# Performance work log

Measured on AMD Instinct MI355X. Metric: run time of the kernel, lower is better.

Reference implementation:

```python
import jax, jax.numpy as jnp
import numpy as np

SCALE = 1.0 / 16.0      # spatial scale: image coords -> feature-map coords (stride-16 backbone)
OUT = 7                 # roi_pool_outsize
RATIO = 2               # sampling_ratio
NUM_CLASSES = 21
HID = 1024
SCORE_THRESH = 0.05
NMS_THRESH = 0.5
DET = 100               # detections_per_img
MIN_SIZE = 0.01
LOG_MAX = float(np.log(1000.0 / 16.0))  # standard bbox decode dw/dh clamp


def _bilinear(feat, ys, xs):
    # feat [C,H,W]; ys [Py], xs [Px] -> [C,Py,Px] (torchvision roi_align interpolation, aligned=False)
    C, H, W = feat.shape
    vy = (ys > -1.0) & (ys < H)
    vx = (xs > -1.0) & (xs < W)
    y = jnp.clip(ys, 0.0, H - 1.0)
    x = jnp.clip(xs, 0.0, W - 1.0)
    y0 = jnp.floor(y).astype(jnp.int32)
    x0 = jnp.floor(x).astype(jnp.int32)
    y1 = jnp.minimum(y0 + 1, H - 1)
    x1 = jnp.minimum(x0 + 1, W - 1)
    ly = (y - y0)[:, None]
    lx = (x - x0)[None, :]
    f00 = feat[:, y0[:, None], x0[None, :]]
    f01 = feat[:, y0[:, None], x1[None, :]]
    f10 = feat[:, y1[:, None], x0[None, :]]
    f11 = feat[:, y1[:, None], x1[None, :]]
    val = (f00 * (1.0 - ly) * (1.0 - lx) + f01 * (1.0 - ly) * lx
           + f10 * ly * (1.0 - lx) + f11 * ly * lx)
    return val * (vy[:, None] & vx[None, :])


def _roi_align(features, boxes, bidx):
    # features [N,C,H,W], boxes [R,4] (image coords), bidx [R] -> [R,C,OUT,OUT]
    N, C, H, W = features.shape
    b = boxes * SCALE
    rw = jnp.maximum(b[:, 2] - b[:, 0], 1.0)
    rh = jnp.maximum(b[:, 3] - b[:, 1], 1.0)
    bw = rw / OUT
    bh = rh / OUT
    # per-bin sample offsets: (ph + (i+0.5)/ratio) for ph in [0,OUT), i in [0,RATIO)
    g = (jnp.arange(OUT, dtype=jnp.float32)[:, None]
         + (jnp.arange(RATIO, dtype=jnp.float32)[None, :] + 0.5) / RATIO).reshape(-1)  # [OUT*RATIO]
    ys = b[:, 1][:, None] + g[None, :] * bh[:, None]  # [R, OUT*RATIO]
    xs = b[:, 0][:, None] + g[None, :] * bw[:, None]
    vals = jax.vmap(lambda i, yr, xr: _bilinear(features[i], yr, xr))(bidx, ys, xs)  # [R,C,P,P]
    R = boxes.shape[0]
    return vals.reshape(R, C, OUT, RATIO, OUT, RATIO).mean(axis=(3, 5))


def _decode(deltas, props):
    # deltas [R,K,4], props [R,4]; weights (10,10,5,5) as in the module
    pw = props[:, 2] - props[:, 0]
    ph = props[:, 3] - props[:, 1]
    pcx = props[:, 0] + 0.5 * pw
    pcy = props[:, 1] + 0.5 * ph
    dx = deltas[..., 0] / 10.0
    dy = deltas[..., 1] / 10.0
    dw = jnp.minimum(deltas[..., 2] / 5.0, LOG_MAX)
    dh = jnp.minimum(deltas[..., 3] / 5.0, LOG_MAX)
    cx = dx * pw[:, None] + pcx[:, None]
    cy = dy * ph[:, None] + pcy[:, None]
    w = jnp.exp(dw) * pw[:, None]
    h = jnp.exp(dh) * ph[:, None]
    return jnp.stack([cx - 0.5 * w, cy - 0.5 * h, cx + 0.5 * w, cy + 0.5 * h], axis=-1)


def _per_image(scores, boxes, img):
    # scores [S,K], boxes [S,K,4]. Drop background class, flatten, filter, class-aware NMS, top-DET.
    S, K = scores.shape
    sc = scores[:, 1:].reshape(-1)                 # [M]
    bx = boxes[:, 1:, :].reshape(-1, 4)            # [M,4]
    lb = jnp.broadcast_to(jnp.arange(1, K, dtype=jnp.int32)[None, :], (S, K - 1)).reshape(-1)
    wv = bx[:, 2] - bx[:, 0]
    hv = bx[:, 3] - bx[:, 1]
    valid = (sc > SCORE_THRESH) & (wv >= MIN_SIZE) & (hv >= MIN_SIZE)
    live0 = jnp.where(valid, sc, -1.0)
    # batched_nms via per-class coordinate offsets
    nb = bx + (lb.astype(bx.dtype) * (img + 1.0))[:, None]
    areas = (nb[:, 2] - nb[:, 0]) * (nb[:, 3] - nb[:, 1])

    def step(live, _):
        i = jnp.argmax(live)
        s = live[i]
        b = nb[i]
        xx1 = jnp.maximum(b[0], nb[:, 0])
        yy1 = jnp.maximum(b[1], nb[:, 1])
        xx2 = jnp.minimum(b[2], nb[:, 2])
        yy2 = jnp.minimum(b[3], nb[:, 3])
        inter = jnp.maximum(xx2 - xx1, 0.0) * jnp.maximum(yy2 - yy1, 0.0)
        area_i = (b[2] - b[0]) * (b[3] - b[1])
        iou = inter / (area_i + areas - inter + 1e-9)
        live = jnp.where(iou > NMS_THRESH, -1.0, live)  # also suppresses i itself (iou=1)
        return live, (i, s)

    _, (idxs, svals) = jax.lax.scan(step, live0, None, length=DET)
    keep = svals > SCORE_THRESH
    out_boxes = jnp.where(keep[:, None], bx[idxs], 0.0)
    out_scores = jnp.where(keep, svals, 0.0)
    out_labels = jnp.where(keep, lb[idxs], 0)
    return out_boxes, out_scores, out_labels


def _forward(features, proposals, w1, b1, w2, b2, wc, bc, wb, bb, image_size):
    N, C, H, W = features.shape
    S = proposals.shape[1]
    props = proposals.reshape(-1, 4)
    bidx = jnp.repeat(jnp.arange(N), S)
    feats = _roi_align(features, props, bidx)          # [R,C,7,7]
    x = feats.reshape(N * S, -1)                       # [R, C*49]
    h = jax.nn.relu(x @ w1 + b1)
    h = jax.nn.relu(h @ w2 + b2)
    cls = h @ wc + bc                                  # [R,K]
    deltas = (h @ wb + bb).reshape(N * S, NUM_CLASSES, 4)
    scores = jax.nn.softmax(cls, axis=-1)
    boxes = _decode(deltas, props)                     # [R,K,4]
    img = float(image_size)
    boxes = jnp.clip(boxes, 0.0, img)                  # square image -> clip both coords to [0,img]
    scores = scores.reshape(N, S, NUM_CLASSES)
    boxes = boxes.reshape(N, S, NUM_CLASSES, 4)
    return jax.vmap(lambda s, bx: _per_image(s, bx, img))(scores, boxes)


def setup_inputs() -> dict:
    key = jax.random.key(0)
    ks = jax.random.split(key, 12)
    N, S, C, H, W = 2, 512, 512, 50, 50
    IMG = 800
    features = jax.random.normal(ks[0], (N, C, H, W), jnp.float32)
    x1 = jax.random.uniform(ks[1], (N, S)) * (IMG - 80.0)
    y1 = jax.random.uniform(ks[2], (N, S)) * (IMG - 80.0)
    x2 = jnp.minimum(x1 + 16.0 + jax.random.uniform(ks[3], (N, S)) * 180.0, float(IMG))
    y2 = jnp.minimum(y1 + 16.0 + jax.random.uniform(ks[4], (N, S)) * 180.0, float(IMG))
    proposals = jnp.stack([x1, y1, x2, y2], axis=-1)
    D = C * OUT * OUT  # 25088
    w1 = jax.random.normal(ks[5], (D, HID), jnp.float32) * 0.01
    b1 = jnp.zeros((HID,), jnp.float32)
    w2 = jax.random.normal(ks[6], (HID, HID), jnp.float32) * 0.02
    b2 = jnp.zeros((HID,), jnp.float32)
    wc = jax.random.normal(ks[7], (HID, NUM_CLASSES), jnp.float32) * 0.05
    bc = jnp.zeros((NUM_CLASSES,), jnp.float32)
    wb = jax.random.normal(ks[8], (HID, NUM_CLASSES * 4), jnp.float32) * 0.02
    bb = jnp.zeros((NUM_CLASSES * 4,), jnp.float32)
    return {"features": features, "proposals": proposals, "w1": w1, "b1": b1,
            "w2": w2, "b2": b2, "wc": wc, "bc": bc, "wb": wb, "bb": bb,
            "image_size": IMG}


def reference(features, proposals, w1, b1, w2, b2, wc, bc, wb, bb, image_size):
    boxes, scores, labels = _forward(features, proposals, w1, b1, w2, b2, wc, bc, wb, bb, image_size)
    return boxes, scores, labels
```

## Files before the change

kernel.cpp:

```cpp
#include <hip/hip_runtime.h>
#include <cmath>

#define NIMG 2
#define SPROP 512
#define NROI 1024
#define CCH 512
#define FH 50
#define FW 50
#define K1 25088
#define HID 1024
#define NCLS 21
#define NDET 100
#define IMGSZ 800.0f
#define LOGMAX 4.135166556742356f
#define MCAND 10240
#define ZSPLIT 8
#define KCHUNK 3136
#define ZSPLIT2 8
#define KCHUNK2 128

typedef unsigned short u16;
typedef __attribute__((ext_vector_type(8))) short short8;
typedef __attribute__((ext_vector_type(4))) float f32x4;
typedef __attribute__((ext_vector_type(16))) float f32x16;

__device__ __forceinline__ u16 f2bf(float x) {
  unsigned int u = __float_as_uint(x);
  u += 0x7fffu + ((u >> 16) & 1u);
  return (u16)(u >> 16);
}
__device__ __forceinline__ float bf2f(u16 h) {
  return __uint_as_float(((unsigned int)h) << 16);
}

__device__ __forceinline__ void gld16(const u16* g, u16* l) {
  __builtin_amdgcn_global_load_lds(
      (const __attribute__((address_space(1))) void*)g,
      (__attribute__((address_space(3))) void*)l, 16, 0, 0);
}

template <bool BF16OUT>
__global__ __launch_bounds__(256) void roi_kernel(
    const float* __restrict__ feat, const float* __restrict__ props,
    float* __restrict__ X, u16* __restrict__ Xhi, u16* __restrict__ Xlo) {
  const int r = blockIdx.x;
  const int n = r >> 9;
  const int tid = threadIdx.x;
  __shared__ float tile[32 * 273 + 16];
  __shared__ float4 ymeta[14];
  __shared__ float4 xmeta[14];
  __shared__ int smin[2];

  const float p0 = props[r * 4 + 0] * 0.0625f;
  const float p1 = props[r * 4 + 1] * 0.0625f;
  const float p2 = props[r * 4 + 2] * 0.0625f;
  const float p3 = props[r * 4 + 3] * 0.0625f;
  const float bw = fmaxf(p2 - p0, 1.0f) / 7.0f;
  const float bh = fmaxf(p3 - p1, 1.0f) / 7.0f;

  if (tid < 14) {
    const int j = tid;
    const float g = (float)(j >> 1) + ((float)(j & 1) + 0.5f) * 0.5f;
    const float y = p1 + g * bh;
    const float vy = (y > -1.0f && y < (float)FH) ? 0.5f : 0.0f;
    const float yc = fminf(fmaxf(y, 0.0f), (float)(FH - 1));
    const int y0 = (int)floorf(yc);
    const int y1 = min(y0 + 1, FH - 1);
    const float ly = yc - (float)y0;
    const float yc0 = fminf(fmaxf(p1 + 0.25f * bh, 0.0f), (float)(FH - 1));
    const int ymin = (int)floorf(yc0);
    float4 m;
    m.x = __int_as_float((y0 - ymin) * 17);
    m.y = __int_as_float((y1 - ymin) * 17);
    m.z = (1.0f - ly) * vy;
    m.w = ly * vy;
    ymeta[j] = m;
    if (j == 0) smin[0] = ymin;
  } else if (tid >= 16 && tid < 30) {
    const int j = tid - 16;
    const float g = (float)(j >> 1) + ((float)(j & 1) + 0.5f) * 0.5f;
    const float x = p0 + g * bw;
    const float vx = (x > -1.0f && x < (float)FW) ? 0.5f : 0.0f;
    const float xc = fminf(fmaxf(x, 0.0f), (float)(FW - 1));
    const int x0 = (int)floorf(xc);
    const int x1 = min(x0 + 1, FW - 1);
    const float lx = xc - (float)x0;
    const float xc0 = fminf(fmaxf(p0 + 0.25f * bw, 0.0f), (float)(FW - 1));
    const int xmin = (int)floorf(xc0);
    const float wx0 = (1.0f - lx) * vx;
    const float wx1 = lx * vx;
    const int d = x1 - x0;
    float4 m;
    m.x = __int_as_float(x0 - xmin);
    m.y = wx0 + (d ? 0.0f : wx1);
    m.z = d ? wx1 : 0.0f;
    m.w = 0.0f;
    xmeta[j] = m;
    if (j == 0) smin[1] = xmin;
  }
  __syncthreads();

  const int ymin = smin[0], xmin = smin[1];
  const float* fb = feat + (size_t)n * CCH * (FH * FW);
  const int gy = min(ymin + (tid >> 4), FH - 1);
  const int gx = min(xmin + (tid & 15), FW - 1);
  const int offp = gy * FW + gx;
  const int wslot = (tid >> 4) * 17 + (tid & 15);
  const int q = tid & 7;
  const int c = tid >> 3;
  const int cb = c * 273;

  float pf[32];
#pragma unroll
  for (int e = 0; e < 32; ++e) pf[e] = fb[(size_t)e * (FH * FW) + offp];

  for (int cc = 0; cc < 16; ++cc) {
#pragma unroll
    for (int e = 0; e < 32; ++e) tile[e * 273 + wslot] = pf[e];
    __syncthreads();
    if (cc < 15) {
      const float* fb2 = fb + (size_t)(cc + 1) * 32 * (FH * FW);
#pragma unroll
      for (int e = 0; e < 32; ++e) pf[e] = fb2[(size_t)e * (FH * FW) + offp];
    }
#pragma unroll
    for (int jj = 0; jj < 7; ++jj) {
      const int s = q + (jj << 3);
      if (s < 49) {
        const int oy = s / 7;
        const int ox = s - oy * 7;
        const float4 ym0 = ymeta[2 * oy];
        const float4 ym1 = ymeta[2 * oy + 1];
        const float4 xm0 = xmeta[2 * ox];
        const float4 xm1 = xmeta[2 * ox + 1];
        float acc = 0.0f;
#pragma unroll
        for (int sy = 0; sy < 2; ++sy) {
          const float4 ym = sy ? ym1 : ym0;
          const int ro0 = cb + __float_as_int(ym.x);
          const int ro1 = cb + __float_as_int(ym.y);
#pragma unroll
          for (int sx = 0; sx < 2; ++sx) {
            const float4 xm = sx ? xm1 : xm0;
            const int px = __float_as_int(xm.x);
            const float a0 = tile[ro0 + px];
            const float a1 = tile[ro0 + px + 1];
            const float b0 = tile[ro1 + px];
            const float b1 = tile[ro1 + px + 1];
            acc += ym.z * (xm.y * a0 + xm.z * a1) +
                   ym.w * (xm.y * b0 + xm.z * b1);
          }
        }
        const size_t k = (size_t)r * K1 + (size_t)(cc * 32 + c) * 49 + s;
        if (BF16OUT) {
          const u16 h = f2bf(acc);
          Xhi[k] = h;
          Xlo[k] = f2bf(acc - bf2f(h));
        } else {
          X[k] = acc;
        }
      }
    }
    __syncthreads();
  }
}

template <int KDIM>
__global__ __launch_bounds__(256) void convw_kernel(
    const float* __restrict__ w, u16* __restrict__ Wh, u16* __restrict__ Wl) {
  __shared__ u16 sh[64][65], sl[64][65];
  const int k0 = blockIdx.x * 64;
  const int n0 = blockIdx.y * 64;
  const int t = threadIdx.x;
#pragma unroll
  for (int e = 0; e < 16; ++e) {
    const int idx = t + e * 256;
    const int kl = idx >> 6, nl = idx & 63;
    const float v = w[(size_t)(k0 + kl) * HID + n0 + nl];
    const u16 h = f2bf(v);
    sh[kl][nl] = h;
    sl[kl][nl] = f2bf(v - bf2f(h));
  }
  __syncthreads();
#pragma unroll
  for (int e = 0; e < 16; ++e) {
    const int idx = t + e * 256;
    const int nl = idx >> 6, kl = idx & 63;
    Wh[(size_t)(n0 + nl) * KDIM + k0 + kl] = sh[kl][nl];
    Wl[(size_t)(n0 + nl) * KDIM + k0 + kl] = sl[kl][nl];
  }
}

template <int KS, int KCH, bool SWZ>
__global__ __launch_bounds__(512, 2) void gemm_mfma_split(
    const u16* __restrict__ Ahg, const u16* __restrict__ Alg,
    const u16* __restrict__ Bhg, const u16* __restrict__ Blg,
    float* __restrict__ CP) {
  __shared__ u16 Ah[2][128][32], Al[2][128][32];
  __shared__ u16 Bh[2][256][32], Bl[2][256][32];
  const int tid = threadIdx.x;
  const int lane = tid & 63;
  const int wv = tid >> 6;
  const int wm = (wv >> 2) << 6;
  const int wn = (wv & 3) << 6;

  int bx = blockIdx.x, by = blockIdx.y, bz = blockIdx.z;
  if (SWZ) {
    const int f = blockIdx.x + ((blockIdx.y + (blockIdx.z << 3)) << 2);
    bz = f & 7;
    const int u = f >> 3;
    bx = u & 3;
    by = u >> 2;
  }
  const int mT = by << 7;
  const int nT = bx << 8;
  const int kz = bz * KCH;
  constexpr int NSTEP = KCH / 32;

  const int sr = tid >> 2;
  const int sqw = (((tid & 3) ^ ((tid >> 3) & 3)) << 3);
  const size_t aoff  = (size_t)(mT + sr) * KS + sqw;
  const size_t b0off = (size_t)(nT + sr) * KS + sqw;
  const size_t b1off = (size_t)(nT + sr + 128) * KS + sqw;
  const int lofs = tid * 8;

  f32x16 acc[2][2];
#pragma unroll
  for (int i = 0; i < 2; ++i)
#pragma unroll
    for (int j = 0; j < 2; ++j)
#pragma unroll
      for (int e = 0; e < 16; ++e) acc[i][j][e] = 0.0f;

  const int fm = lane & 31;
  const int fh = lane >> 5;
  const int vswz = (fm >> 1) & 3;

  auto stage = [&](int buf, int kb) {
    gld16(Ahg + aoff + kb, &Ah[buf][0][0] + lofs);
    gld16(Alg + aoff + kb, &Al[buf][0][0] + lofs);
    gld16(Bhg + b0off + kb, &Bh[buf][0][0] + lofs);
    gld16(Bhg + b1off + kb, &Bh[buf][128][0] + lofs);
    gld16(Blg + b0off + kb, &Bl[buf][0][0] + lofs);
    gld16(Blg + b1off + kb, &Bl[buf][128][0] + lofs);
  };

  auto compute = [&](int buf) {
#pragma unroll
    for (int kh = 0; kh < 2; ++kh) {
      const int cA = ((((kh << 1) | fh) ^ vswz) << 3);
      short8 fa_h[2], fa_l[2], fb_h[2], fb_l[2];
#pragma unroll
      for (int t = 0; t < 2; ++t) {
        fa_h[t] = *(const short8*)(&Ah[buf][wm + t * 32 + fm][cA]);
        fa_l[t] = *(const short8*)(&Al[buf][wm + t * 32 + fm][cA]);
        fb_h[t] = *(const short8*)(&Bh[buf][wn + t * 32 + fm][cA]);
        fb_l[t] = *(const short8*)(&Bl[buf][wn + t * 32 + fm][cA]);
      }
#pragma unroll
      for (int ti = 0; ti < 2; ++ti)
#pragma unroll
        for (int tj = 0; tj < 2; ++tj) {
          acc[ti][tj] = __builtin_amdgcn_mfma_f32_32x32x16_bf16(
              fa_h[ti], fb_h[tj], acc[ti][tj], 0, 0, 0);
          acc[ti][tj] = __builtin_amdgcn_mfma_f32_32x32x16_bf16(
              fa_h[ti], fb_l[tj], acc[ti][tj], 0, 0, 0);
          acc[ti][tj] = __builtin_amdgcn_mfma_f32_32x32x16_bf16(
              fa_l[ti], fb_h[tj], acc[ti][tj], 0, 0, 0);
        }
    }
  };

  stage(0, kz);
  asm volatile("s_waitcnt vmcnt(0)" ::: "memory");
  __builtin_amdgcn_s_barrier();
  __builtin_amdgcn_sched_barrier(0);

  int cur = 0;
  for (int s = 0; s < NSTEP; ++s) {
    if (s + 1 < NSTEP) {
      stage(cur ^ 1, kz + (s + 1) * 32);
      asm volatile("s_waitcnt vmcnt(6)" ::: "memory");
    } else {
      asm volatile("s_waitcnt vmcnt(0)" ::: "memory");
    }
    __builtin_amdgcn_s_barrier();
    __builtin_amdgcn_sched_barrier(0);
    compute(cur);
    __builtin_amdgcn_sched_barrier(0);
    __builtin_amdgcn_s_barrier();
    cur ^= 1;
  }

  float* Cp = CP + (size_t)bz * ((size_t)NROI * HID);
  const int ccol = nT + wn + fm;
  const int rbase = mT + wm + (fh << 2);
#pragma unroll
  for (int ti = 0; ti < 2; ++ti)
#pragma unroll
    for (int tj = 0; tj < 2; ++tj)
#pragma unroll
      for (int rg = 0; rg < 16; ++rg) {
        const int row = rbase + ti * 32 + (rg & 3) + 8 * (rg >> 2);
        Cp[(size_t)row * HID + ccol + tj * 32] = acc[ti][tj][rg];
      }
}

__global__ __launch_bounds__(256) void gemm1_kernel(
    const float* __restrict__ A, const float* __restrict__ B,
    float* __restrict__ CP) {
  __shared__ float As[16][68];
  __shared__ float Bs[16][68];
  const int tid = threadIdx.x;
  const int mTile = blockIdx.y << 6;
  const int nTile = blockIdx.x << 6;
  const int k0 = blockIdx.z * KCHUNK;
  const int ty = tid >> 4, tx = tid & 15;
  const int ar = tid >> 2, ac = (tid & 3) << 2;
  const int br = tid >> 4, bcl = (tid & 15) << 2;
  float acc[4][4] = {};

  for (int kb = k0; kb < k0 + KCHUNK; kb += 16) {
    const float4 av = *(const float4*)(A + (size_t)(mTile + ar) * K1 + kb + ac);
    const float4 bv = *(const float4*)(B + (size_t)(kb + br) * HID + nTile + bcl);
    As[ac + 0][ar] = av.x; As[ac + 1][ar] = av.y;
    As[ac + 2][ar] = av.z; As[ac + 3][ar] = av.w;
    *(float4*)(&Bs[br][bcl]) = bv;
    __syncthreads();
#pragma unroll
    for (int kk = 0; kk < 16; ++kk) {
      const float4 a4 = *(const float4*)(&As[kk][ty << 2]);
      const float4 b4 = *(const float4*)(&Bs[kk][tx << 2]);
      const float aa[4] = {a4.x, a4.y, a4.z, a4.w};
      const float bb4[4] = {b4.x, b4.y, b4.z, b4.w};
#pragma unroll
      for (int i = 0; i < 4; ++i)
#pragma unroll
        for (int j = 0; j < 4; ++j)
          acc[i][j] = fmaf(aa[i], bb4[j], acc[i][j]);
    }
    __syncthreads();
  }
  float* Cp = CP + (size_t)blockIdx.z * (HID * NROI);
#pragma unroll
  for (int i = 0; i < 4; ++i) {
    *(float4*)(Cp + (size_t)(mTile + (ty << 2) + i) * HID + nTile + (tx << 2)) =
        make_float4(acc[i][0], acc[i][1], acc[i][2], acc[i][3]);
  }
}

__global__ __launch_bounds__(256) void bias_relu_bf16_kernel(
    const float* __restrict__ CP, const float* __restrict__ b1,
    u16* __restrict__ H1h, u16* __restrict__ H1l) {
  const int idx = blockIdx.x * 256 + threadIdx.x;
  float v = b1[idx & (HID - 1)];
#pragma unroll
  for (int z = 0; z < ZSPLIT; ++z) v += CP[(size_t)z * (HID * NROI) + idx];
  v = fmaxf(v, 0.0f);
  const u16 h = f2bf(v);
  H1h[idx] = h;
  H1l[idx] = f2bf(v - bf2f(h));
}

__global__ __launch_bounds__(256) void bias_relu_f32_kernel(
    const float* __restrict__ CP, const float* __restrict__ b1,
    float* __restrict__ H1) {
  const int idx = blockIdx.x * 256 + threadIdx.x;
  float v = b1[idx & (HID - 1)];
#pragma unroll
  for (int z = 0; z < ZSPLIT; ++z) v += CP[(size_t)z * (HID * NROI) + idx];
  H1[idx] = fmaxf(v, 0.0f);
}

__global__ __launch_bounds__(256) void bias_relu2_kernel(
    const float* __restrict__ CP2, const float* __restrict__ b2,
    float* __restrict__ H2) {
  const int idx = blockIdx.x * 256 + threadIdx.x;
  float v = b2[idx & (HID - 1)];
#pragma unroll
  for (int z = 0; z < ZSPLIT2; ++z) v += CP2[(size_t)z * (HID * NROI) + idx];
  H2[idx] = fmaxf(v, 0.0f);
}

__global__ __launch_bounds__(256) void gemm2_kernel(
    const float* __restrict__ A, const float* __restrict__ B,
    const float* __restrict__ bias, float* __restrict__ C) {
  __shared__ float As[16][68];
  __shared__ float Bs[16][68];
  const int tid = threadIdx.x;
  const int mTile = blockIdx.y << 6;
  const int nTile = blockIdx.x << 6;
  const int ty = tid >> 4, tx = tid & 15;
  const int ar = tid >> 2, ac = (tid & 3) << 2;
  const int br = tid >> 4, bcl = (tid & 15) << 2;
  float acc[4][4] = {};

  for (int kb = 0; kb < HID; kb += 16) {
    const float4 av = *(const float4*)(A + (size_t)(mTile + ar) * HID + kb + ac);
    const float4 bv = *(const float4*)(B + (size_t)(kb + br) * HID + nTile + bcl);
    As[ac + 0][ar] = av.x; As[ac + 1][ar] = av.y;
    As[ac + 2][ar] = av.z; As[ac + 3][ar] = av.w;
    *(float4*)(&Bs[br][bcl]) = bv;
    __syncthreads();
#pragma unroll
    for (int kk = 0; kk < 16; ++kk) {
      const float4 a4 = *(const float4*)(&As[kk][ty << 2]);
      const float4 b4 = *(const float4*)(&Bs[kk][tx << 2]);
      const float aa[4] = {a4.x, a4.y, a4.z, a4.w};
      const float bb4[4] = {b4.x, b4.y, b4.z, b4.w};
#pragma unroll
      for (int i = 0; i < 4; ++i)
#pragma unroll
        for (int j = 0; j < 4; ++j)
          acc[i][j] = fmaf(aa[i], bb4[j], acc[i][j]);
    }
    __syncthreads();
  }
#pragma unroll
  for (int i = 0; i < 4; ++i) {
#pragma unroll
    for (int j = 0; j < 4; ++j) {
      float v = acc[i][j] + bias[nTile + (tx << 2) + j];
      acc[i][j] = fmaxf(v, 0.0f);
    }
    *(float4*)(C + (size_t)(mTile + (ty << 2) + i) * HID + nTile + (tx << 2)) =
        make_float4(acc[i][0], acc[i][1], acc[i][2], acc[i][3]);
  }
}

__global__ __launch_bounds__(128) void heads_kernel(
    const float* __restrict__ H2m, const float* __restrict__ wc,
    const float* __restrict__ bc, const float* __restrict__ wb,
    const float* __restrict__ bb, const float* __restrict__ props,
    float* __restrict__ BX2, float* __restrict__ NB2,
    float* __restrict__ LV2) {
  const int r = blockIdx.x;
  const int tid = threadIdx.x;
  __shared__ float hrow[HID];
  __shared__ float vals[112];
  __shared__ float red[2];

  for (int i = tid; i < HID; i += 128) hrow[i] = H2m[(size_t)r * HID + i];
  __syncthreads();

  if (tid < 105) {
    float acc;
    if (tid < NCLS) {
      acc = bc[tid];
      for (int kk = 0; kk < HID; ++kk) acc = fmaf(hrow[kk], wc[kk * NCLS + tid], acc);
    } else {
      const int j = tid - NCLS;
      acc = bb[j];
      for (int kk = 0; kk < HID; ++kk) acc = fmaf(hrow[kk], wb[kk * (NCLS * 4) + j], acc);
    }
    vals[tid] = acc;
  }
  __syncthreads();

  if (tid == 0) {
    float m = vals[0];
    for (int k = 1; k < NCLS; ++k) m = fmaxf(m, vals[k]);
    float s = 0.0f;
    for (int k = 0; k < NCLS; ++k) s += expf(vals[k] - m);
    red[0] = m;
    red[1] = 1.0f / s;
  }
  __syncthreads();

  if (tid >= 1 && tid <= 20) {
    const int k = tid;
    const float prob = expf(vals[k] - red[0]) * red[1];

    const float px1 = props[r * 4 + 0], py1 = props[r * 4 + 1];
    const float px2 = props[r * 4 + 2], py2 = props[r * 4 + 3];
    const float pw = px2 - px1, ph = py2 - py1;
    const float pcx = px1 + 0.5f * pw, pcy = py1 + 0.5f * ph;

    const float dx = vals[NCLS + k * 4 + 0] / 10.0f;
    const float dy = vals[NCLS + k * 4 + 1] / 10.0f;
    const float dw = fminf(vals[NCLS + k * 4 + 2] / 5.0f, LOGMAX);
    const float dh = fminf(vals[NCLS + k * 4 + 3] / 5.0f, LOGMAX);

    const float cx = dx * pw + pcx, cy = dy * ph + pcy;
    const float w = expf(dw) * pw, h = expf(dh) * ph;
    float b0 = cx - 0.5f * w, b1c = cy - 0.5f * h;
    float b2 = cx + 0.5f * w, b3 = cy + 0.5f * h;
    b0 = fminf(fmaxf(b0, 0.0f), IMGSZ);
    b1c = fminf(fmaxf(b1c, 0.0f), IMGSZ);
    b2 = fminf(fmaxf(b2, 0.0f), IMGSZ);
    b3 = fminf(fmaxf(b3, 0.0f), IMGSZ);

    const float wv = b2 - b0, hv = b3 - b1c;
    const bool valid = (prob > 0.05f) && (wv >= 0.01f) && (hv >= 0.01f);

    const int n = r >> 9, s = r & 511;
    const int cand = (k - 1) * SPROP + s;
    const size_t bi = (size_t)n * MCAND + cand;
    const float off = (float)k * (IMGSZ + 1.0f);

    BX2[bi * 4 + 0] = b0; BX2[bi * 4 + 1] = b1c;
    BX2[bi * 4 + 2] = b2; BX2[bi * 4 + 3] = b3;
    NB2[bi * 4 + 0] = b0 + off; NB2[bi * 4 + 1] = b1c + off;
    NB2[bi * 4 + 2] = b2 + off; NB2[bi * 4 + 3] = b3 + off;
    LV2[bi] = valid ? prob : -1.0f;
  }
}

template <int CTRL>
__device__ __forceinline__ void red2(float& v, int& ix) {
  const float tv = __int_as_float(__builtin_amdgcn_update_dpp(
      (int)0xC0000000, __float_as_int(v), CTRL, 0xf, 0xf, false));
  const int ti = __builtin_amdgcn_update_dpp(0x7fffffff, ix, CTRL, 0xf, 0xf, false);
  if (tv > v || (tv == v && ti < ix)) { v = tv; ix = ti; }
}
__device__ __forceinline__ void wave_red2(float& v, int& ix) {
  red2<0x111>(v, ix);
  red2<0x112>(v, ix);
  red2<0x114>(v, ix);
  red2<0x118>(v, ix);
  red2<0x142>(v, ix);
  red2<0x143>(v, ix);
}

__global__ __launch_bounds__(64) void nms_class_kernel(
    const float* __restrict__ NB2, const float* __restrict__ LV2,
    float* __restrict__ ksg, int* __restrict__ kig, int* __restrict__ cntg) {
  const int bid = blockIdx.x;
  const int lane = threadIdx.x;
  __shared__ float4 lbox[SPROP];
  const size_t cb = (size_t)bid * SPROP;

  float lv[8], b0[8], b1[8], b2[8], b3[8], ar[8];
#pragma unroll
  for (int j = 0; j < 8; ++j) {
    const int s = lane + j * 64;
    lv[j] = LV2[cb + s];
    const float4 b = *(const float4*)(NB2 + (cb + s) * 4);
    b0[j] = b.x; b1[j] = b.y; b2[j] = b.z; b3[j] = b.w;
    ar[j] = (b.z - b.x) * (b.w - b.y);
    lbox[s] = b;
  }

  int cnt = 0;
  for (int d = 0; d < NDET; ++d) {
    float bv = -2.0f;
    int bix = 0x7fffffff;
#pragma unroll
    for (int j = 0; j < 8; ++j) {
      if (lv[j] > bv) { bv = lv[j]; bix = lane + j * 64; }
    }
    wave_red2(bv, bix);
    const float bv2 = __shfl(bv, 63);
    const int bix2 = __shfl(bix, 63);
    if (bv2 <= 0.05f) break;

    if (lane == 0) {
      ksg[bid * NDET + cnt] = bv2;
      kig[bid * NDET + cnt] = bix2;
    }
    ++cnt;

    const float4 wb = lbox[bix2];
    const float wa = (wb.z - wb.x) * (wb.w - wb.y);
#pragma unroll
    for (int j = 0; j < 8; ++j) {
      const float xx1 = fmaxf(wb.x, b0[j]);
      const float yy1 = fmaxf(wb.y, b1[j]);
      const float xx2 = fminf(wb.z, b2[j]);
      const float yy2 = fminf(wb.w, b3[j]);
      const float inter = fmaxf(xx2 - xx1, 0.0f) * fmaxf(yy2 - yy1, 0.0f);
      const float iou = inter / (wa + ar[j] - inter + 1e-9f);
      if (iou > 0.5f) lv[j] = -1.0f;
    }
  }
  if (lane == 0) cntg[bid] = cnt;
}

__global__ __launch_bounds__(1024) void nms_merge_kernel(
    const float* __restrict__ ksg, const int* __restrict__ kig,
    const int* __restrict__ cntg, const float* __restrict__ BX2,
    float* __restrict__ out) {
  const int n = blockIdx.x;
  const int tid = threadIdx.x;
  __shared__ int cbase[21];
  __shared__ unsigned long long keys[2000];
  __shared__ float ssc[2000];
  __shared__ int sfl[2000];
  __shared__ float svals[NDET];
  __shared__ int sflat[NDET];

  if (tid == 0) {
    int acc = 0;
    for (int c = 0; c < 20; ++c) { cbase[c] = acc; acc += cntg[n * 20 + c]; }
    cbase[20] = acc;
  }
  __syncthreads();
  const int T = cbase[20];

  for (int idx = tid; idx < 20 * NDET; idx += 1024) {
    const int c = idx / NDET, e = idx - (idx / NDET) * NDET;
    if (e < cntg[n * 20 + c]) {
      const int pos = cbase[c] + e;
      const float s = ksg[(n * 20 + c) * NDET + e];
      const int slot = kig[(n * 20 + c) * NDET + e];
      const int flat = slot * 20 + c;
      ssc[pos] = s;
      sfl[pos] = flat;
      keys[pos] = ((unsigned long long)__float_as_uint(s) << 32) |
                  (unsigned long long)(0xFFFFFFFFu - (unsigned)flat);
    }
  }
  __syncthreads();

  float msc[2]; int mfl[2]; unsigned long long mk[2]; int rank[2] = {0, 0};
  bool own[2];
#pragma unroll
  for (int e = 0; e < 2; ++e) {
    const int i = tid + e * 1024;
    own[e] = (i < T);
    if (own[e]) { mk[e] = keys[i]; msc[e] = ssc[i]; mfl[e] = sfl[i]; }
  }
  for (int i = 0; i < T; ++i) {
    const unsigned long long k = keys[i];
    if (own[0] && k > mk[0]) ++rank[0];
    if (own[1] && k > mk[1]) ++rank[1];
  }
#pragma unroll
  for (int e = 0; e < 2; ++e)
    if (own[e] && rank[e] < NDET) { svals[rank[e]] = msc[e]; sflat[rank[e]] = mfl[e]; }
  __syncthreads();

  if (tid < NDET) {
    const int m = (T < NDET) ? T : NDET;
    const bool keep = tid < m;
    float sv = 0.0f;
    float4 bx4 = make_float4(0.0f, 0.0f, 0.0f, 0.0f);
    float label = 0.0f;
    if (keep) {
      sv = svals[tid];
      const int flat = sflat[tid];
      const int c = flat % 20, s = flat / 20;
      bx4 = *(const float4*)(BX2 + ((size_t)(n * 20 + c) * SPROP + s) * 4);
      label = (float)(c + 1);
    }
    out[(n * NDET + tid) * 4 + 0] = bx4.x;
    out[(n * NDET + tid) * 4 + 1] = bx4.y;
    out[(n * NDET + tid) * 4 + 2] = bx4.z;
    out[(n * NDET + tid) * 4 + 3] = bx4.w;
    out[NIMG * NDET * 4 + n * NDET + tid] = sv;
    out[NIMG * NDET * 4 + NIMG * NDET + n * NDET + tid] = label;
  }
}

extern "C" void kernel_launch(void* const* d_in, const int* in_sizes, int n_in,
                              void* d_out, int out_size, void* d_ws, size_t ws_size,
                              hipStream_t stream) {
  const float* features  = (const float*)d_in[0];
  const float* proposals = (const float*)d_in[1];
  const float* w1 = (const float*)d_in[2];
  const float* b1 = (const float*)d_in[3];
  const float* w2 = (const float*)d_in[4];
  const float* b2 = (const float*)d_in[5];
  const float* wc = (const float*)d_in[6];
  const float* bc = (const float*)d_in[7];
  const float* wb = (const float*)d_in[8];
  const float* bb = (const float*)d_in[9];

  const size_t XE = (size_t)NROI * K1;
  const size_t WE = (size_t)K1 * HID;
  const size_t FLOATS_TAIL =
      (size_t)ZSPLIT * NROI * HID + 2 * (size_t)NROI * HID + (size_t)NIMG * MCAND * 10;
  const size_t NEED = (XE * 2 + WE * 2) * sizeof(u16) + FLOATS_TAIL * sizeof(float);

  if (ws_size >= NEED) {
    u16* Xhi = (u16*)d_ws;
    u16* Xlo = Xhi + XE;
    u16* Wh  = Xlo + XE;
    u16* Wl  = Wh + WE;
    float* CP  = (float*)(Wl + WE);
    float* CP2 = CP;
    float* H2  = CP + (size_t)ZSPLIT * NROI * HID;
    float* BX2 = H2 + (size_t)NROI * HID;
    float* NB2 = BX2 + (size_t)NIMG * MCAND * 4;
    float* LV2 = NB2 + (size_t)NIMG * MCAND * 4;
    float* ksg = LV2 + (size_t)NIMG * MCAND;
    int*   kig = (int*)(ksg + (size_t)NIMG * 20 * NDET);
    int*   cntg = kig + (size_t)NIMG * 20 * NDET;
    u16* H1h = Xhi;
    u16* H1l = Xhi + (size_t)NROI * HID;
    u16* W2h = Xlo;
    u16* W2l = Xlo + (size_t)HID * HID;

    convw_kernel<K1><<<dim3(K1 / 64, HID / 64), 256, 0, stream>>>(w1, Wh, Wl);
    roi_kernel<true><<<NROI, 256, 0, stream>>>(features, proposals, nullptr, Xhi, Xlo);
    gemm_mfma_split<K1, KCHUNK, true><<<dim3(4, 8, ZSPLIT), 512, 0, stream>>>(
        Xhi, Xlo, Wh, Wl, CP);
    bias_relu_bf16_kernel<<<(NROI * HID) / 256, 256, 0, stream>>>(CP, b1, H1h, H1l);
    convw_kernel<HID><<<dim3(HID / 64, HID / 64), 256, 0, stream>>>(w2, W2h, W2l);
    gemm_mfma_split<HID, KCHUNK2, true><<<dim3(4, 8, ZSPLIT2), 512, 0, stream>>>(
        H1h, H1l, W2h, W2l, CP2);
    bias_relu2_kernel<<<(NROI * HID) / 256, 256, 0, stream>>>(CP2, b2, H2);
    heads_kernel<<<NROI, 128, 0, stream>>>(H2, wc, bc, wb, bb, proposals,
                                           BX2, NB2, LV2);
    nms_class_kernel<<<NIMG * 20, 64, 0, stream>>>(NB2, LV2, ksg, kig, cntg);
    nms_merge_kernel<<<NIMG, 1024, 0, stream>>>(ksg, kig, cntg, BX2,
                                                (float*)d_out);
  } else {
    float* ws = (float*)d_ws;
    float* X   = ws;
    float* CP  = X + XE;
    float* H1  = CP + (size_t)ZSPLIT * NROI * HID;
    float* H2  = H1 + (size_t)NROI * HID;
    float* BX2 = H2 + (size_t)NROI * HID;
    float* NB2 = BX2 + (size_t)NIMG * MCAND * 4;
    float* LV2 = NB2 + (size_t)NIMG * MCAND * 4;
    float* ksg = LV2 + (size_t)NIMG * MCAND;
    int*   kig = (int*)(ksg + (size_t)NIMG * 20 * NDET);
    int*   cntg = kig + (size_t)NIMG * 20 * NDET;

    roi_kernel<false><<<NROI, 256, 0, stream>>>(features, proposals, X, nullptr, nullptr);
    gemm1_kernel<<<dim3(16, 16, ZSPLIT), 256, 0, stream>>>(X, w1, CP);
    bias_relu_f32_kernel<<<(NROI * HID) / 256, 256, 0, stream>>>(CP, b1, H1);
    gemm2_kernel<<<dim3(16, 16), 256, 0, stream>>>(H1, w2, b2, H2);
    heads_kernel<<<NROI, 128, 0, stream>>>(H2, wc, bc, wb, bb, proposals,
                                           BX2, NB2, LV2);
    nms_class_kernel<<<NIMG * 20, 64, 0, stream>>>(NB2, LV2, ksg, kig, cntg);
    nms_merge_kernel<<<NIMG, 1024, 0, stream>>>(ksg, kig, cntg, BX2,
                                                (float*)d_out);
  }
}
```

Before: 826.9 us.

## Triple-buffer split GEMM with interleaved staging and MFMA priority phases

Moves the bf16-split MFMA GEMM from double to triple LDS buffering, so global loads are issued two k-steps ahead. The loads are split into two halves interleaved between the two k-half compute phases, and the MFMA bursts run under raised wave priority (s_setprio). The aim is to hide global-load latency behind MFMA work and smooth out issue pressure. In exchange, LDS use grows by half, which may limit the two-blocks-per-CU occupancy, and more barriers are added per step.

```diff
diff --git a/kernel.cpp b/kernel.cpp
--- a/kernel.cpp
+++ b/kernel.cpp
@@ -196,8 +196,8 @@
     const u16* __restrict__ Ahg, const u16* __restrict__ Alg,
     const u16* __restrict__ Bhg, const u16* __restrict__ Blg,
     float* __restrict__ CP) {
-  __shared__ u16 Ah[2][128][32], Al[2][128][32];
-  __shared__ u16 Bh[2][256][32], Bl[2][256][32];
+  __shared__ u16 Ah[3][128][32], Al[3][128][32];
+  __shared__ u16 Bh[3][256][32], Bl[3][256][32];
   const int tid = threadIdx.x;
   const int lane = tid & 63;
   const int wv = tid >> 6;
@@ -236,60 +236,71 @@
   const int fh = lane >> 5;
   const int vswz = (fm >> 1) & 3;
 
-  auto stage = [&](int buf, int kb) {
+  auto stage3a = [&](int buf, int kb) {
     gld16(Ahg + aoff + kb, &Ah[buf][0][0] + lofs);
     gld16(Alg + aoff + kb, &Al[buf][0][0] + lofs);
     gld16(Bhg + b0off + kb, &Bh[buf][0][0] + lofs);
+  };
+  auto stage3b = [&](int buf, int kb) {
     gld16(Bhg + b1off + kb, &Bh[buf][128][0] + lofs);
     gld16(Blg + b0off + kb, &Bl[buf][0][0] + lofs);
     gld16(Blg + b1off + kb, &Bl[buf][128][0] + lofs);
   };
 
-  auto compute = [&](int buf) {
-#pragma unroll
-    for (int kh = 0; kh < 2; ++kh) {
-      const int cA = ((((kh << 1) | fh) ^ vswz) << 3);
-      short8 fa_h[2], fa_l[2], fb_h[2], fb_l[2];
-#pragma unroll
-      for (int t = 0; t < 2; ++t) {
-        fa_h[t] = *(const short8*)(&Ah[buf][wm + t * 32 + fm][cA]);
-        fa_l[t] = *(const short8*)(&Al[buf][wm + t * 32 + fm][cA]);
-        fb_h[t] = *(const short8*)(&Bh[buf][wn + t * 32 + fm][cA]);
-        fb_l[t] = *(const short8*)(&Bl[buf][wn + t * 32 + fm][cA]);
+  auto phase = [&](int buf, int kh, bool st, int stbuf, int stkb, bool half_a) {
+    const int cA = ((((kh << 1) | fh) ^ vswz) << 3);
+    short8 fa_h[2], fa_l[2], fb_h[2], fb_l[2];
+#pragma unroll
+    for (int t = 0; t < 2; ++t) {
+      fa_h[t] = *(const short8*)(&Ah[buf][wm + t * 32 + fm][cA]);
+      fa_l[t] = *(const short8*)(&Al[buf][wm + t * 32 + fm][cA]);
+      fb_h[t] = *(const short8*)(&Bh[buf][wn + t * 32 + fm][cA]);
+      fb_l[t] = *(const short8*)(&Bl[buf][wn + t * 32 + fm][cA]);
+    }
+    if (st) {
+      if (half_a) stage3a(stbuf, stkb);
+      else        stage3b(stbuf, stkb);
+    }
+    __builtin_amdgcn_s_barrier();
+    asm volatile("s_waitcnt lgkmcnt(0)" ::: "memory");
+    __builtin_amdgcn_sched_barrier(0);
+    __builtin_amdgcn_s_setprio(1);
+#pragma unroll
+    for (int ti = 0; ti < 2; ++ti)
+#pragma unroll
+      for (int tj = 0; tj < 2; ++tj) {
+        acc[ti][tj] = __builtin_amdgcn_mfma_f32_32x32x16_bf16(
+            fa_h[ti], fb_h[tj], acc[ti][tj], 0, 0, 0);
+        acc[ti][tj] = __builtin_amdgcn_mfma_f32_32x32x16_bf16(
+            fa_h[ti], fb_l[tj], acc[ti][tj], 0, 0, 0);
+        acc[ti][tj] = __builtin_amdgcn_mfma_f32_32x32x16_bf16(
+            fa_l[ti], fb_h[tj], acc[ti][tj], 0, 0, 0);
       }
-#pragma unroll
-      for (int ti = 0; ti < 2; ++ti)
-#pragma unroll
-        for (int tj = 0; tj < 2; ++tj) {
-          acc[ti][tj] = __builtin_amdgcn_mfma_f32_32x32x16_bf16(
-              fa_h[ti], fb_h[tj], acc[ti][tj], 0, 0, 0);
-          acc[ti][tj] = __builtin_amdgcn_mfma_f32_32x32x16_bf16(
-              fa_h[ti], fb_l[tj], acc[ti][tj], 0, 0, 0);
-          acc[ti][tj] = __builtin_amdgcn_mfma_f32_32x32x16_bf16(
-              fa_l[ti], fb_h[tj], acc[ti][tj], 0, 0, 0);
-        }
-    }
+    __builtin_amdgcn_s_setprio(0);
+    __builtin_amdgcn_sched_barrier(0);
   };
 
-  stage(0, kz);
-  asm volatile("s_waitcnt vmcnt(0)" ::: "memory");
+  stage3a(0, kz);
+  stage3b(0, kz);
+  stage3a(1, kz + 32);
+  stage3b(1, kz + 32);
+  asm volatile("s_waitcnt vmcnt(6)" ::: "memory");
   __builtin_amdgcn_s_barrier();
-  __builtin_amdgcn_sched_barrier(0);
-
-  int cur = 0;
+
+  int c0 = 0, c1 = 1, c2 = 2;
   for (int s = 0; s < NSTEP; ++s) {
-    if (s + 1 < NSTEP) {
-      stage(cur ^ 1, kz + (s + 1) * 32);
+    const int kb2 = kz + (s + 2) * 32;
+    const bool st = (s + 2 < NSTEP);
+    phase(c0, 0, st, c2, kb2, true);
+    __builtin_amdgcn_s_barrier();
+    phase(c0, 1, st, c2, kb2, false);
+    if (st) {
       asm volatile("s_waitcnt vmcnt(6)" ::: "memory");
-    } else {
+    } else if (s + 1 < NSTEP) {
       asm volatile("s_waitcnt vmcnt(0)" ::: "memory");
     }
     __builtin_amdgcn_s_barrier();
-    __builtin_amdgcn_sched_barrier(0);
-    compute(cur);
-    __builtin_amdgcn_sched_barrier(0);
-    __builtin_amdgcn_s_barrier();
-    cur ^= 1;
+    const int t = c0; c0 = c1; c1 = c2; c2 = t;
   }
 
   float* Cp = CP + (size_t)bz * ((size_t)NROI * HID);
```

After: 788.9 us. 1.05x faster.
